# Kernel optimization log

Hardware: AMD Instinct MI355X
Metric: run time of the kernel (lower is better)

Reference implementation:

```python
import jax, jax.numpy as jnp
import numpy as np

EPS = 1e-05

def _rmsnorm(h, w, eps=EPS):
    var = jnp.mean(h * h, axis=-1, keepdims=True)
    return h * jax.lax.rsqrt(var + eps) * w

def setup_inputs() -> dict:
    key = jax.random.key(0)
    ks = jax.random.split(key, 9)
    B, S, H, I, R = 2, 4096, 4096, 14336, 1592
    s_h = 1.0 / np.sqrt(H)
    s_r = 1.0 / np.sqrt(R)
    s_i = 1.0 / np.sqrt(I)
    return {
        "x": jax.random.normal(ks[0], (B, S, H), jnp.float32),
        "residual": jax.random.normal(ks[1], (B, S, H), jnp.float32),
        "ln_w": jnp.ones((H,), jnp.float32),
        "w_gate_v": jax.random.normal(ks[2], (H, R), jnp.float32) * s_h,
        "w_gate_u": jax.random.normal(ks[3], (R, I), jnp.float32) * s_r,
        "w_up_v": jax.random.normal(ks[4], (H, R), jnp.float32) * s_h,
        "w_up_u": jax.random.normal(ks[5], (R, I), jnp.float32) * s_r,
        "w_down_v": jax.random.normal(ks[6], (I, R), jnp.float32) * s_i,
        "w_down_u": jax.random.normal(ks[7], (R, H), jnp.float32) * s_r,
    }

def reference(x, residual, ln_w, w_gate_v, w_gate_u, w_up_v, w_up_u, w_down_v, w_down_u):
    # fused residual add + RMSNorm (as in the fused NKI kernel path)
    h = x + residual                    # [B,S,H]
    n = _rmsnorm(h, ln_w)               # [B,S,H]
    # low-rank gate / up projections: H -> R -> I
    gate = jax.nn.silu(jnp.einsum('bsh,hr,ri->bsi', n, w_gate_v, w_gate_u))
    up = jnp.einsum('bsh,hr,ri->bsi', n, w_up_v, w_up_u)
    # low-rank down projection: I -> R -> H
    out = jnp.einsum('bsi,ir,rh->bsh', gate * up, w_down_v, w_down_u)
    return out
```

## Files before the change

### kernel.cpp

```cpp
#include <hip/hip_runtime.h>
#include <cstdint>
#include <cstddef>

typedef __attribute__((ext_vector_type(8))) short short8;
typedef __attribute__((ext_vector_type(4))) float floatx4;

__device__ __forceinline__ float bf2f(unsigned short u) {
    union { float f; uint32_t i; } v; v.i = ((uint32_t)u) << 16; return v.f;
}
__device__ __forceinline__ unsigned short f2bf(float f) {
    union { float f; uint32_t i; } v; v.f = f;
    uint32_t r = v.i + 0x7FFFu + ((v.i >> 16) & 1u);
    return (unsigned short)(r >> 16);
}

__global__ __launch_bounds__(256)
void add_rmsnorm_kernel(const float* __restrict__ x, const float* __restrict__ res,
                        const float* __restrict__ w, unsigned short* __restrict__ out,
                        int H, float invH)
{
    const size_t row = blockIdx.x;
    const float4* xv = (const float4*)(x + row * (size_t)H);
    const float4* rv = (const float4*)(res + row * (size_t)H);
    const float4* wv = (const float4*)w;
    const int nvec = H >> 2;
    float4 h[8];
    float s = 0.f;
    int cnt = 0;
    for (int idx = threadIdx.x; idx < nvec; idx += 256) {
        float4 a = xv[idx], b = rv[idx];
        float4 hh = make_float4(a.x + b.x, a.y + b.y, a.z + b.z, a.w + b.w);
        h[cnt++] = hh;
        s += hh.x * hh.x + hh.y * hh.y + hh.z * hh.z + hh.w * hh.w;
    }
    __shared__ float red[256];
    red[threadIdx.x] = s;
    __syncthreads();
    for (int off = 128; off > 0; off >>= 1) {
        if (threadIdx.x < off) red[threadIdx.x] += red[threadIdx.x + off];
        __syncthreads();
    }
    const float scale = rsqrtf(red[0] * invH + 1e-5f);
    ushort4* ov = (ushort4*)(out + row * (size_t)H);
    cnt = 0;
    for (int idx = threadIdx.x; idx < nvec; idx += 256) {
        float4 hh = h[cnt++];
        float4 ww = wv[idx];
        ushort4 o;
        o.x = f2bf(hh.x * scale * ww.x);
        o.y = f2bf(hh.y * scale * ww.y);
        o.z = f2bf(hh.z * scale * ww.z);
        o.w = f2bf(hh.w * scale * ww.w);
        ov[idx] = o;
    }
}

__global__ __launch_bounds__(256)
void transpose_cast(const float* __restrict__ src, unsigned short* __restrict__ dst,
                    int P, int Q)
{
    __shared__ float tile[32][33];
    const int qt = blockIdx.x * 32, pt = blockIdx.y * 32;
    const int tx = threadIdx.x, ty = threadIdx.y;
    #pragma unroll
    for (int r = 0; r < 32; r += 8) {
        int p = pt + ty + r, q = qt + tx;
        tile[ty + r][tx] = (p < P && q < Q) ? src[(size_t)p * Q + q] : 0.f;
    }
    __syncthreads();
    #pragma unroll
    for (int r = 0; r < 32; r += 8) {
        int q = qt + ty + r, p = pt + tx;
        if (q < Q && p < P) dst[(size_t)q * P + p] = f2bf(tile[tx][ty + r]);
    }
}

template<int EPI>
__global__ __launch_bounds__(256)
void gemm128(const unsigned short* __restrict__ A,
             const unsigned short* __restrict__ Bt,
             void* __restrict__ Cv,
             const unsigned short* __restrict__ other,
             int M, int N, int K)
{
    __shared__ unsigned short As[128 * 40];
    __shared__ unsigned short Bs[128 * 40];
    const int tid  = threadIdx.x;
    const int m0   = blockIdx.y << 7;
    const int n0   = blockIdx.x << 7;
    const int lane = tid & 63;
    const int wave = tid >> 6;
    const int quad = lane >> 4;
    const int lr   = lane & 15;
    const int wm   = (wave >> 1) << 6;
    const int wn   = (wave & 1) << 6;

    const floatx4 zero = {0.f, 0.f, 0.f, 0.f};
    floatx4 acc[4][4];
    #pragma unroll
    for (int i = 0; i < 4; i++)
        #pragma unroll
        for (int j = 0; j < 4; j++) acc[i][j] = zero;

    const int r0  = tid >> 2;
    const int kc0 = (tid & 3) << 3;

    for (int k0 = 0; k0 < K; k0 += 32) {
        const bool kok = (k0 + kc0 + 8) <= K;
        uint4 av0 = {0,0,0,0}, av1 = {0,0,0,0}, bv0 = {0,0,0,0}, bv1 = {0,0,0,0};
        if (kok) {
            av0 = *(const uint4*)(A + (size_t)(m0 + r0) * K + k0 + kc0);
            av1 = *(const uint4*)(A + (size_t)(m0 + r0 + 64) * K + k0 + kc0);
            if (n0 + r0 < N)
                bv0 = *(const uint4*)(Bt + (size_t)(n0 + r0) * K + k0 + kc0);
            if (n0 + r0 + 64 < N)
                bv1 = *(const uint4*)(Bt + (size_t)(n0 + r0 + 64) * K + k0 + kc0);
        }
        *(uint4*)(As + (r0)      * 40 + kc0) = av0;
        *(uint4*)(As + (r0 + 64) * 40 + kc0) = av1;
        *(uint4*)(Bs + (r0)      * 40 + kc0) = bv0;
        *(uint4*)(Bs + (r0 + 64) * 40 + kc0) = bv1;
        __syncthreads();

        short8 af[4], bfr[4];
        #pragma unroll
        for (int mi = 0; mi < 4; mi++)
            af[mi] = *(const short8*)(As + (wm + mi * 16 + lr) * 40 + quad * 8);
        #pragma unroll
        for (int ni = 0; ni < 4; ni++)
            bfr[ni] = *(const short8*)(Bs + (wn + ni * 16 + lr) * 40 + quad * 8);
        #pragma unroll
        for (int mi = 0; mi < 4; mi++)
            #pragma unroll
            for (int ni = 0; ni < 4; ni++)
                acc[mi][ni] = __builtin_amdgcn_mfma_f32_16x16x32_bf16(
                    af[mi], bfr[ni], acc[mi][ni], 0, 0, 0);
        __syncthreads();
    }

    #pragma unroll
    for (int mi = 0; mi < 4; mi++) {
        const int growb = m0 + wm + mi * 16 + quad * 4;
        #pragma unroll
        for (int ni = 0; ni < 4; ni++) {
            const int col = n0 + wn + ni * 16 + lr;
            if (col < N) {
                #pragma unroll
                for (int i = 0; i < 4; i++) {
                    const size_t idx = (size_t)(growb + i) * N + col;
                    const float v = acc[mi][ni][i];
                    if (EPI == 0) {
                        ((unsigned short*)Cv)[idx] = f2bf(v);
                    } else if (EPI == 1) {
                        ((float*)Cv)[idx] = v;
                    } else {
                        const float o = bf2f(other[idx]);
                        const float sg = v / (1.f + __expf(-v));
                        ((unsigned short*)Cv)[idx] = f2bf(sg * o);
                    }
                }
            }
        }
    }
}

extern "C" void kernel_launch(void* const* d_in, const int* in_sizes, int n_in,
                              void* d_out, int out_size, void* d_ws, size_t ws_size,
                              hipStream_t stream)
{
    const float* x   = (const float*)d_in[0];
    const float* res = (const float*)d_in[1];
    const float* lnw = (const float*)d_in[2];
    const float* wgv = (const float*)d_in[3];
    const float* wgu = (const float*)d_in[4];
    const float* wuv = (const float*)d_in[5];
    const float* wuu = (const float*)d_in[6];
    const float* wdv = (const float*)d_in[7];
    const float* wdu = (const float*)d_in[8];

    const int H = in_sizes[2];
    const int T = (int)((long long)in_sizes[0] / H);
    const int R = in_sizes[3] / H;
    const int I = in_sizes[4] / R;

    unsigned short* p = (unsigned short*)d_ws;
    unsigned short* Wgv_t = p; p += (size_t)R * H;
    unsigned short* Wuv_t = p; p += (size_t)R * H;
    unsigned short* Wgu_t = p; p += (size_t)I * R;
    unsigned short* Wuu_t = p; p += (size_t)I * R;
    unsigned short* Wdv_t = p; p += (size_t)R * I;
    unsigned short* Wdu_t = p; p += (size_t)H * R;
    unsigned short* nbuf  = p; p += (size_t)T * H;
    unsigned short* g1    = p; p += (size_t)T * R;
    unsigned short* u1    = p; p += (size_t)T * R;
    unsigned short* upm   = p; p += (size_t)T * I;
    unsigned short* d1    = nbuf;

    dim3 tb(32, 8);
    transpose_cast<<<dim3((R + 31) / 32, (H + 31) / 32), tb, 0, stream>>>(wgv, Wgv_t, H, R);
    transpose_cast<<<dim3((R + 31) / 32, (H + 31) / 32), tb, 0, stream>>>(wuv, Wuv_t, H, R);
    transpose_cast<<<dim3((I + 31) / 32, (R + 31) / 32), tb, 0, stream>>>(wgu, Wgu_t, R, I);
    transpose_cast<<<dim3((I + 31) / 32, (R + 31) / 32), tb, 0, stream>>>(wuu, Wuu_t, R, I);
    transpose_cast<<<dim3((R + 31) / 32, (I + 31) / 32), tb, 0, stream>>>(wdv, Wdv_t, I, R);
    transpose_cast<<<dim3((H + 31) / 32, (R + 31) / 32), tb, 0, stream>>>(wdu, Wdu_t, R, H);

    add_rmsnorm_kernel<<<T, 256, 0, stream>>>(x, res, lnw, nbuf, H, 1.0f / (float)H);

    dim3 gR((R + 127) / 128, T / 128);
    dim3 gI((I + 127) / 128, T / 128);
    dim3 gH((H + 127) / 128, T / 128);

    gemm128<0><<<gR, 256, 0, stream>>>(nbuf, Wgv_t, g1, nullptr, T, R, H);
    gemm128<0><<<gR, 256, 0, stream>>>(nbuf, Wuv_t, u1, nullptr, T, R, H);
    gemm128<0><<<gI, 256, 0, stream>>>(u1, Wuu_t, upm, nullptr, T, I, R);
    gemm128<2><<<gI, 256, 0, stream>>>(g1, Wgu_t, upm, upm, T, I, R);
    gemm128<0><<<gR, 256, 0, stream>>>(upm, Wdv_t, d1, nullptr, T, R, I);
    gemm128<1><<<gH, 256, 0, stream>>>(d1, Wdu_t, d_out, nullptr, T, H, R);
}
```

Before: 3.375 ms.

## Use direct global-to-LDS loads, pad rank to 64, and swizzle blocks across XCDs

The GEMM tile loads now use the global_load_lds builtin to copy straight into shared memory without going through registers. The low-rank dimension R is zero-padded to a multiple of 64 in the weights and intermediates, which removes the per-load bounds checks. A 1D grid with an XCD-aware block swizzle is added to improve L2 locality. The LDS row stride drops its padding from 40 to 32, which may bring back bank conflicts on the fragment reads, and padding adds a little extra compute.

```diff
diff --git a/kernel.cpp b/kernel.cpp
--- a/kernel.cpp
+++ b/kernel.cpp
@@ -12,6 +12,20 @@
     union { float f; uint32_t i; } v; v.f = f;
     uint32_t r = v.i + 0x7FFFu + ((v.i >> 16) & 1u);
     return (unsigned short)(r >> 16);
+}
+
+__device__ __forceinline__ void gl_lds16(const unsigned short* g, unsigned short* l) {
+    __builtin_amdgcn_global_load_lds(
+        (const __attribute__((address_space(1))) unsigned int*)g,
+        (__attribute__((address_space(3))) unsigned int*)l,
+        16, 0, 0);
+}
+
+__device__ __forceinline__ int xcd_swizzle(int bid, int nwg) {
+    const int nx = 8;
+    const int q = nwg / nx, r = nwg % nx;
+    const int xcd = bid % nx, local = bid / nx;
+    return (xcd < r ? xcd * (q + 1) : r * (q + 1) + (xcd - r) * q) + local;
 }
 
 __global__ __launch_bounds__(256)
@@ -57,7 +71,7 @@
 
 __global__ __launch_bounds__(256)
 void transpose_cast(const float* __restrict__ src, unsigned short* __restrict__ dst,
-                    int P, int Q)
+                    int P, int Q, int Pld, int Qld)
 {
     __shared__ float tile[32][33];
     const int qt = blockIdx.x * 32, pt = blockIdx.y * 32;
@@ -71,7 +85,7 @@
     #pragma unroll
     for (int r = 0; r < 32; r += 8) {
         int q = qt + ty + r, p = pt + tx;
-        if (q < Q && p < P) dst[(size_t)q * P + p] = f2bf(tile[tx][ty + r]);
+        if (q < Qld && p < Pld) dst[(size_t)q * Pld + p] = f2bf(tile[tx][ty + r]);
     }
 }
 
@@ -81,13 +95,14 @@
              const unsigned short* __restrict__ Bt,
              void* __restrict__ Cv,
              const unsigned short* __restrict__ other,
-             int M, int N, int K)
-{
-    __shared__ unsigned short As[128 * 40];
-    __shared__ unsigned short Bs[128 * 40];
+             int N, int Nld, int K, int gx)
+{
+    __shared__ unsigned short As[128 * 32];
+    __shared__ unsigned short Bs[128 * 32];
     const int tid  = threadIdx.x;
-    const int m0   = blockIdx.y << 7;
-    const int n0   = blockIdx.x << 7;
+    const int bid  = xcd_swizzle(blockIdx.x, gridDim.x);
+    const int n0   = (bid % gx) << 7;
+    const int m0   = (bid / gx) << 7;
     const int lane = tid & 63;
     const int wave = tid >> 6;
     const int quad = lane >> 4;
@@ -102,33 +117,35 @@
         #pragma unroll
         for (int j = 0; j < 4; j++) acc[i][j] = zero;
 
-    const int r0  = tid >> 2;
-    const int kc0 = (tid & 3) << 3;
+    const int lrow = lane >> 2;
+    const int lk8  = (lane & 3) << 3;
+
+    unsigned short* lA0 = As + (wave * 32) * 32;
+    unsigned short* lA1 = lA0 + 16 * 32;
+    unsigned short* lB0 = Bs + (wave * 32) * 32;
+    unsigned short* lB1 = lB0 + 16 * 32;
+
+    const unsigned short* gA0 = A + (size_t)(m0 + wave * 32 + lrow) * K + lk8;
+    const unsigned short* gA1 = gA0 + (size_t)16 * K;
+    int rb0 = n0 + wave * 32 + lrow;      if (rb0 >= Nld) rb0 = 0;
+    int rb1 = n0 + wave * 32 + 16 + lrow; if (rb1 >= Nld) rb1 = 0;
+    const unsigned short* gB0 = Bt + (size_t)rb0 * K + lk8;
+    const unsigned short* gB1 = Bt + (size_t)rb1 * K + lk8;
 
     for (int k0 = 0; k0 < K; k0 += 32) {
-        const bool kok = (k0 + kc0 + 8) <= K;
-        uint4 av0 = {0,0,0,0}, av1 = {0,0,0,0}, bv0 = {0,0,0,0}, bv1 = {0,0,0,0};
-        if (kok) {
-            av0 = *(const uint4*)(A + (size_t)(m0 + r0) * K + k0 + kc0);
-            av1 = *(const uint4*)(A + (size_t)(m0 + r0 + 64) * K + k0 + kc0);
-            if (n0 + r0 < N)
-                bv0 = *(const uint4*)(Bt + (size_t)(n0 + r0) * K + k0 + kc0);
-            if (n0 + r0 + 64 < N)
-                bv1 = *(const uint4*)(Bt + (size_t)(n0 + r0 + 64) * K + k0 + kc0);
-        }
-        *(uint4*)(As + (r0)      * 40 + kc0) = av0;
-        *(uint4*)(As + (r0 + 64) * 40 + kc0) = av1;
-        *(uint4*)(Bs + (r0)      * 40 + kc0) = bv0;
-        *(uint4*)(Bs + (r0 + 64) * 40 + kc0) = bv1;
+        gl_lds16(gA0 + k0, lA0);
+        gl_lds16(gA1 + k0, lA1);
+        gl_lds16(gB0 + k0, lB0);
+        gl_lds16(gB1 + k0, lB1);
         __syncthreads();
 
         short8 af[4], bfr[4];
         #pragma unroll
         for (int mi = 0; mi < 4; mi++)
-            af[mi] = *(const short8*)(As + (wm + mi * 16 + lr) * 40 + quad * 8);
+            af[mi] = *(const short8*)(As + (wm + mi * 16 + lr) * 32 + quad * 8);
         #pragma unroll
         for (int ni = 0; ni < 4; ni++)
-            bfr[ni] = *(const short8*)(Bs + (wn + ni * 16 + lr) * 40 + quad * 8);
+            bfr[ni] = *(const short8*)(Bs + (wn + ni * 16 + lr) * 32 + quad * 8);
         #pragma unroll
         for (int mi = 0; mi < 4; mi++)
             #pragma unroll
@@ -144,13 +161,13 @@
         #pragma unroll
         for (int ni = 0; ni < 4; ni++) {
             const int col = n0 + wn + ni * 16 + lr;
-            if (col < N) {
+            if (col < Nld) {
                 #pragma unroll
                 for (int i = 0; i < 4; i++) {
-                    const size_t idx = (size_t)(growb + i) * N + col;
+                    const size_t idx = (size_t)(growb + i) * Nld + col;
                     const float v = acc[mi][ni][i];
                     if (EPI == 0) {
-                        ((unsigned short*)Cv)[idx] = f2bf(v);
+                        ((unsigned short*)Cv)[idx] = (col < N) ? f2bf(v) : (unsigned short)0;
                     } else if (EPI == 1) {
                         ((float*)Cv)[idx] = v;
                     } else {
@@ -182,38 +199,40 @@
     const int T = (int)((long long)in_sizes[0] / H);
     const int R = in_sizes[3] / H;
     const int I = in_sizes[4] / R;
+    const int Rp = (R + 63) & ~63;
 
     unsigned short* p = (unsigned short*)d_ws;
-    unsigned short* Wgv_t = p; p += (size_t)R * H;
-    unsigned short* Wuv_t = p; p += (size_t)R * H;
-    unsigned short* Wgu_t = p; p += (size_t)I * R;
-    unsigned short* Wuu_t = p; p += (size_t)I * R;
-    unsigned short* Wdv_t = p; p += (size_t)R * I;
-    unsigned short* Wdu_t = p; p += (size_t)H * R;
+    unsigned short* Wgv_t = p; p += (size_t)Rp * H;
+    unsigned short* Wuv_t = p; p += (size_t)Rp * H;
+    unsigned short* Wgu_t = p; p += (size_t)I * Rp;
+    unsigned short* Wuu_t = p; p += (size_t)I * Rp;
+    unsigned short* Wdv_t = p; p += (size_t)Rp * I;
+    unsigned short* Wdu_t = p; p += (size_t)H * Rp;
     unsigned short* nbuf  = p; p += (size_t)T * H;
-    unsigned short* g1    = p; p += (size_t)T * R;
-    unsigned short* u1    = p; p += (size_t)T * R;
+    unsigned short* g1    = p; p += (size_t)T * Rp;
+    unsigned short* u1    = p; p += (size_t)T * Rp;
     unsigned short* upm   = p; p += (size_t)T * I;
     unsigned short* d1    = nbuf;
 
     dim3 tb(32, 8);
-    transpose_cast<<<dim3((R + 31) / 32, (H + 31) / 32), tb, 0, stream>>>(wgv, Wgv_t, H, R);
-    transpose_cast<<<dim3((R + 31) / 32, (H + 31) / 32), tb, 0, stream>>>(wuv, Wuv_t, H, R);
-    transpose_cast<<<dim3((I + 31) / 32, (R + 31) / 32), tb, 0, stream>>>(wgu, Wgu_t, R, I);
-    transpose_cast<<<dim3((I + 31) / 32, (R + 31) / 32), tb, 0, stream>>>(wuu, Wuu_t, R, I);
-    transpose_cast<<<dim3((R + 31) / 32, (I + 31) / 32), tb, 0, stream>>>(wdv, Wdv_t, I, R);
-    transpose_cast<<<dim3((H + 31) / 32, (R + 31) / 32), tb, 0, stream>>>(wdu, Wdu_t, R, H);
+    transpose_cast<<<dim3((Rp + 31) / 32, (H + 31) / 32), tb, 0, stream>>>(wgv, Wgv_t, H, R, H, Rp);
+    transpose_cast<<<dim3((Rp + 31) / 32, (H + 31) / 32), tb, 0, stream>>>(wuv, Wuv_t, H, R, H, Rp);
+    transpose_cast<<<dim3((I + 31) / 32, (Rp + 31) / 32), tb, 0, stream>>>(wgu, Wgu_t, R, I, Rp, I);
+    transpose_cast<<<dim3((I + 31) / 32, (Rp + 31) / 32), tb, 0, stream>>>(wuu, Wuu_t, R, I, Rp, I);
+    transpose_cast<<<dim3((Rp + 31) / 32, (I + 31) / 32), tb, 0, stream>>>(wdv, Wdv_t, I, R, I, Rp);
+    transpose_cast<<<dim3((H + 31) / 32, (Rp + 31) / 32), tb, 0, stream>>>(wdu, Wdu_t, R, H, Rp, H);
 
     add_rmsnorm_kernel<<<T, 256, 0, stream>>>(x, res, lnw, nbuf, H, 1.0f / (float)H);
 
-    dim3 gR((R + 127) / 128, T / 128);
-    dim3 gI((I + 127) / 128, T / 128);
-    dim3 gH((H + 127) / 128, T / 128);
-
-    gemm128<0><<<gR, 256, 0, stream>>>(nbuf, Wgv_t, g1, nullptr, T, R, H);
-    gemm128<0><<<gR, 256, 0, stream>>>(nbuf, Wuv_t, u1, nullptr, T, R, H);
-    gemm128<0><<<gI, 256, 0, stream>>>(u1, Wuu_t, upm, nullptr, T, I, R);
-    gemm128<2><<<gI, 256, 0, stream>>>(g1, Wgu_t, upm, upm, T, I, R);
-    gemm128<0><<<gR, 256, 0, stream>>>(upm, Wdv_t, d1, nullptr, T, R, I);
-    gemm128<1><<<gH, 256, 0, stream>>>(d1, Wdu_t, d_out, nullptr, T, H, R);
-}
+    const int gxR = (Rp + 127) / 128;
+    const int gxI = (I + 127) / 128;
+    const int gxH = (H + 127) / 128;
+    const int gy  = T / 128;
+
+    gemm128<0><<<gxR * gy, 256, 0, stream>>>(nbuf, Wgv_t, g1, nullptr, R, Rp, H, gxR);
+    gemm128<0><<<gxR * gy, 256, 0, stream>>>(nbuf, Wuv_t, u1, nullptr, R, Rp, H, gxR);
+    gemm128<0><<<gxI * gy, 256, 0, stream>>>(u1, Wuu_t, upm, nullptr, I, I, Rp, gxI);
+    gemm128<2><<<gxI * gy, 256, 0, stream>>>(g1, Wgu_t, upm, upm, I, I, Rp, gxI);
+    gemm128<0><<<gxR * gy, 256, 0, stream>>>(upm, Wdv_t, d1, nullptr, R, Rp, I, gxR);
+    gemm128<1><<<gxH * gy, 256, 0, stream>>>(d1, Wdu_t, d_out, nullptr, H, H, Rp, gxH);
+}
```

After: 3.081 ms. 1.1x faster.
